# Optimization experiments

Measured on AMD Instinct MI355X. Metric: run time of the kernel, lower is better.

Reference implementation:

```python
import jax, jax.numpy as jnp
import numpy as np

B, V, F, N = 4, 8192, 16384, 8192
EPS = 1e-3        # criterion eps
WEIGHT = 1000.0   # criterion weight


def setup_inputs() -> dict:
    key = jax.random.key(0)
    k1, k2, k3 = jax.random.split(key, 3)
    pred_pos = jax.random.normal(k1, (B, N, 3), jnp.float32)
    obstacle_pos = jax.random.normal(k2, (B, V, 3), jnp.float32)
    obstacle_faces = jax.random.randint(k3, (B, F, 3), 0, V)
    return {"pred_pos": pred_pos, "obstacle_pos": obstacle_pos,
            "obstacle_faces": obstacle_faces}


def _centers_normals(pos, faces):
    # pos: [V,3], faces: [F,3] -> face centers [F,3], unit face normals [F,3]
    tri = pos[faces]                                   # [F,3,3]
    centers = tri.mean(axis=1)                         # gather(...).mean(-2)
    n = jnp.cross(tri[:, 1] - tri[:, 0], tri[:, 2] - tri[:, 0])
    n = n / jnp.maximum(jnp.linalg.norm(n, axis=-1, keepdims=True), 1e-12)
    return centers, n


def reference(pred_pos, obstacle_pos, obstacle_faces):
    centers, normals = jax.vmap(_centers_normals)(obstacle_pos, obstacle_faces)
    # brute-force 1-NN: argmin_f ||p - c_f||^2 == argmin_f (||c_f||^2 - 2 p.c_f)
    c2 = jnp.sum(centers * centers, axis=-1)                     # [B,F]
    dots = jnp.einsum('bnd,bfd->bnf', pred_pos, centers)         # [B,N,F] big
    nn_idx = jnp.argmin(c2[:, None, :] - 2.0 * dots, axis=-1)    # [B,N]
    idx3 = jnp.broadcast_to(nn_idx[:, :, None], nn_idx.shape + (3,))
    nn_points = jnp.take_along_axis(centers, idx3, axis=1)       # [B,N,3]
    nn_normals = jnp.take_along_axis(normals, idx3, axis=1)      # [B,N,3]
    distance = jnp.sum((pred_pos - nn_points) * nn_normals, axis=-1)  # [B,N]
    interp = jnp.maximum(EPS - distance, 0.0)
    perc = jnp.mean((interp > 0).astype(jnp.float32))            # mean over B of per-example means (equal N)
    loss = jnp.mean(jnp.sum(interp ** 3, axis=-1)) * WEIGHT      # sum_i loss_i / B * weight
    return loss, perc
```

## Files before the change

### kernel.cpp

```cpp
#include <hip/hip_runtime.h>
#include <cstdint>

typedef __attribute__((ext_vector_type(8))) short short8;
typedef __attribute__((ext_vector_type(4))) float floatx4;

constexpr int NB = 4;
constexpr int NV = 8192;
constexpr int NF = 16384;
constexpr int NP = 8192;
constexpr float F_EPS = 1e-3f;
constexpr float F_WEIGHT = 1000.0f;
constexpr float BIAS = 1e-3f;

constexpr int PT_TILES = NP / 16;
constexpr int FC_TILES = NF / 16;
constexpr int TPB = 256;
constexpr int TPW = 4;
constexpr int FS = 8;
constexpr int SL_TILES = FC_TILES / FS;
constexpr int CH_TILES = 32;
constexpr int NCHUNK = SL_TILES / CH_TILES;

union FragU { uint4 u; short8 s; };

__device__ inline unsigned f2bf(float f) {
    unsigned u = __float_as_uint(f);
    return (u + 0x7FFFu + ((u >> 16) & 1u)) >> 16;
}
__device__ inline float bf2f(unsigned h) { return __uint_as_float(h << 16); }
__device__ inline unsigned pk(unsigned lo, unsigned hi) {
    return (lo & 0xFFFFu) | (hi << 16);
}

__global__ void points_prep(const float* __restrict__ pred,
                            uint4* __restrict__ a_frags,
                            unsigned* __restrict__ keys,
                            float* __restrict__ acc) {
    int i = blockIdx.x * blockDim.x + threadIdx.x;
    if (i >= NB * NP) return;
    keys[i] = 0xFFFFFFFFu;
    if (i < 2) acc[i] = 0.0f;

    int b = i / NP, n = i & (NP - 1);
    float x = pred[3 * (size_t)i], y = pred[3 * (size_t)i + 1], z = pred[3 * (size_t)i + 2];
    unsigned hx = f2bf(x), hy = f2bf(y), hz = f2bf(z);
    float rx = x - bf2f(hx), ry = y - bf2f(hy), rz = z - bf2f(hz);
    unsigned ahx = f2bf(-2.f * bf2f(hx)), ahy = f2bf(-2.f * bf2f(hy)), ahz = f2bf(-2.f * bf2f(hz));
    unsigned alx = f2bf(-2.f * rx), aly = f2bf(-2.f * ry), alz = f2bf(-2.f * rz);
    float p2 = x * x + y * y + z * z + BIAS;
    unsigned p2h = f2bf(p2);
    unsigned p2l = f2bf(p2 - bf2f(p2h));
    const unsigned ONE = 0x3F80u;

    int tile = n >> 4, m = n & 15;
    uint4* base = a_frags + (size_t)(b * PT_TILES + tile) * 64;
    base[m]      = make_uint4(pk(ahx, ahy), pk(ahz, alx), pk(aly, alz), pk(ahx, ahy));
    base[16 + m] = make_uint4(pk(ahz, alx), pk(aly, alz), pk(ONE, ONE), pk(p2h, p2l));
    base[32 + m] = make_uint4(0, 0, 0, 0);
    base[48 + m] = make_uint4(0, 0, 0, 0);
}

__global__ void faces_prep(const float* __restrict__ pos,
                           const int*   __restrict__ faces,
                           uint4*  __restrict__ b_frags,
                           float4* __restrict__ centers4,
                           float4* __restrict__ normals4) {
    int i = blockIdx.x * blockDim.x + threadIdx.x;
    if (i >= NB * NF) return;
    int b = i / NF, f = i & (NF - 1);
    const float* p = pos + (size_t)b * NV * 3;
    int i0 = faces[3 * (size_t)i], i1 = faces[3 * (size_t)i + 1], i2 = faces[3 * (size_t)i + 2];
    float ax = p[3 * i0], ay = p[3 * i0 + 1], az = p[3 * i0 + 2];
    float bx = p[3 * i1], by = p[3 * i1 + 1], bz = p[3 * i1 + 2];
    float cx = p[3 * i2], cy = p[3 * i2 + 1], cz = p[3 * i2 + 2];

    const float third = 1.0f / 3.0f;
    float mx = (ax + bx + cx) * third;
    float my = (ay + by + cy) * third;
    float mz = (az + bz + cz) * third;
    float c2 = mx * mx + my * my + mz * mz;

    float e1x = bx - ax, e1y = by - ay, e1z = bz - az;
    float e2x = cx - ax, e2y = cy - ay, e2z = cz - az;
    float nx = e1y * e2z - e1z * e2y;
    float ny = e1z * e2x - e1x * e2z;
    float nz = e1x * e2y - e1y * e2x;
    float len = sqrtf(nx * nx + ny * ny + nz * nz);
    float inv = 1.0f / fmaxf(len, 1e-12f);

    centers4[i] = make_float4(mx, my, mz, c2);
    normals4[i] = make_float4(nx * inv, ny * inv, nz * inv, 0.0f);

    unsigned bhx = f2bf(mx), bhy = f2bf(my), bhz = f2bf(mz);
    unsigned blx = f2bf(mx - bf2f(bhx)), bly = f2bf(my - bf2f(bhy)), blz = f2bf(mz - bf2f(bhz));
    unsigned c2h = f2bf(c2);
    unsigned c2l = f2bf(c2 - bf2f(c2h));
    const unsigned ONE = 0x3F80u;

    int tile = f >> 4, m = f & 15;
    uint4* base = b_frags + (size_t)(b * FC_TILES + tile) * 64;
    base[m]      = make_uint4(pk(bhx, bhy), pk(bhz, bhx), pk(bhy, bhz), pk(blx, bly));
    base[16 + m] = make_uint4(pk(blz, blx), pk(bly, blz), pk(c2h, c2l), pk(ONE, ONE));
    base[32 + m] = make_uint4(0, 0, 0, 0);
    base[48 + m] = make_uint4(0, 0, 0, 0);
}

__global__ __launch_bounds__(TPB) void nn_kernel(
        const uint4* __restrict__ a_frags,
        const uint4* __restrict__ b_frags,
        unsigned* __restrict__ keys) {
    __shared__ uint4 sb[CH_TILES * 64];

    const int pg   = blockIdx.x;
    const int sl   = blockIdx.y;
    const int b    = blockIdx.z;
    const int tid  = threadIdx.x;
    const int wave = tid >> 6;
    const int lane = tid & 63;
    const int col  = lane & 15;

    FragU a[TPW];
    const int base_t = b * PT_TILES + pg * 16 + wave * TPW;
#pragma unroll
    for (int t = 0; t < TPW; ++t)
        a[t].u = a_frags[(size_t)(base_t + t) * 64 + lane];

    unsigned best[TPW * 4];
#pragma unroll
    for (int e = 0; e < TPW * 4; ++e) best[e] = 0xFFFFFFFFu;

    const floatx4 zero = {0.f, 0.f, 0.f, 0.f};

    for (int ch = 0; ch < NCHUNK; ++ch) {
        const size_t g0 = (size_t)(b * FC_TILES + sl * SL_TILES + ch * CH_TILES) * 64;
        for (int idx = tid; idx < CH_TILES * 64; idx += TPB)
            sb[idx] = b_frags[g0 + idx];
        __syncthreads();

        unsigned vface = (unsigned)(sl * (SL_TILES * 16) + ch * (CH_TILES * 16) + col);
        for (int t = 0; t < CH_TILES; ++t) {
            FragU bu;
            bu.u = sb[t * 64 + lane];
#pragma unroll
            for (int tt = 0; tt < TPW; ++tt) {
                floatx4 d = __builtin_amdgcn_mfma_f32_16x16x32_bf16(
                    a[tt].s, bu.s, zero, 0, 0, 0);
#pragma unroll
                for (int r = 0; r < 4; ++r) {
                    unsigned key = (__float_as_uint(d[r]) & 0xFFFFC000u) | vface;
                    best[tt * 4 + r] = min(best[tt * 4 + r], key);
                }
            }
            vface += 16;
        }
        __syncthreads();
    }

#pragma unroll
    for (int e = 0; e < TPW * 4; ++e) {
        unsigned v = best[e];
#pragma unroll
        for (int m = 1; m < 16; m <<= 1)
            v = min(v, (unsigned)__shfl_xor((int)v, m, 64));
        best[e] = v;
    }
    if (col == 0) {
        int q = lane >> 4;
#pragma unroll
        for (int tt = 0; tt < TPW; ++tt)
#pragma unroll
            for (int r = 0; r < 4; ++r) {
                int n = (pg * 16 + wave * TPW + tt) * 16 + q * 4 + r;
                atomicMin(&keys[b * NP + n], best[tt * 4 + r]);
            }
    }
}

__global__ __launch_bounds__(TPB) void finalize_kernel(
        const float* __restrict__ pred,
        const float4* __restrict__ centers4,
        const float4* __restrict__ normals4,
        const unsigned int* __restrict__ keys,
        float* __restrict__ acc) {
    int i = blockIdx.x * blockDim.x + threadIdx.x;
    float val = 0.0f, cnt = 0.0f;
    if (i < NB * NP) {
        int b = i / NP;
        unsigned key = keys[i];
        int idx = (int)(key & (unsigned)(NF - 1));
        float4 c  = centers4[b * NF + idx];
        float4 nr = normals4[b * NF + idx];
        const float* pp = pred + (size_t)i * 3;
        float dx = pp[0] - c.x, dy = pp[1] - c.y, dz = pp[2] - c.z;
        float dist = dx * nr.x + dy * nr.y + dz * nr.z;
        float t = F_EPS - dist;
        if (t > 0.0f) { cnt = 1.0f; val = t * t * t; }
    }
    for (int off = 32; off > 0; off >>= 1) {
        val += __shfl_down(val, off, 64);
        cnt += __shfl_down(cnt, off, 64);
    }
    __shared__ float sv[TPB / 64], sn[TPB / 64];
    int lane = threadIdx.x & 63, wave = threadIdx.x >> 6;
    if (lane == 0) { sv[wave] = val; sn[wave] = cnt; }
    __syncthreads();
    if (threadIdx.x == 0) {
        float v = 0.0f, cc = 0.0f;
#pragma unroll
        for (int w = 0; w < TPB / 64; ++w) { v += sv[w]; cc += sn[w]; }
        atomicAdd(&acc[0], v);
        atomicAdd(&acc[1], cc);
    }
}

__global__ void out_kernel(const float* __restrict__ acc,
                           float* __restrict__ out) {
    if (threadIdx.x == 0) {
        out[0] = acc[0] * (F_WEIGHT / (float)NB);
        out[1] = acc[1] * (1.0f / (float)(NB * NP));
    }
}

extern "C" void kernel_launch(void* const* d_in, const int* in_sizes, int n_in,
                              void* d_out, int out_size, void* d_ws, size_t ws_size,
                              hipStream_t stream) {
    const float* pred  = (const float*)d_in[0];
    const float* opos  = (const float*)d_in[1];
    const int*   faces = (const int*)  d_in[2];

    char* ws = (char*)d_ws;
    const size_t a_bytes = (size_t)NB * PT_TILES * 64 * 16;
    const size_t b_bytes = (size_t)NB * FC_TILES * 64 * 16;
    const size_t c_bytes = (size_t)NB * NF * 16;

    uint4*    a_frags  = (uint4*)ws;
    uint4*    b_frags  = (uint4*)(ws + a_bytes);
    float4*   centers4 = (float4*)(ws + a_bytes + b_bytes);
    float4*   normals4 = (float4*)(ws + a_bytes + b_bytes + c_bytes);
    unsigned* keys     = (unsigned*)(ws + a_bytes + b_bytes + 2 * c_bytes);
    float*    acc      = (float*)(ws + a_bytes + b_bytes + 2 * c_bytes +
                                  (size_t)NB * NP * sizeof(unsigned));

    points_prep<<<(NB * NP + TPB - 1) / TPB, TPB, 0, stream>>>(
        pred, a_frags, keys, acc);
    faces_prep<<<(NB * NF + TPB - 1) / TPB, TPB, 0, stream>>>(
        opos, faces, b_frags, centers4, normals4);

    nn_kernel<<<dim3(NP / 256, FS, NB), TPB, 0, stream>>>(
        a_frags, b_frags, keys);

    finalize_kernel<<<(NB * NP + TPB - 1) / TPB, TPB, 0, stream>>>(
        pred, centers4, normals4, keys, acc);

    out_kernel<<<1, 64, 0, stream>>>(acc, (float*)d_out);
}
```

Measured before the change: 124.1 us.

## Fuse prep kernels, drop LDS staging, fold finalize into NN kernel via tickets

```diff
diff --git a/kernel.cpp b/kernel.cpp
--- a/kernel.cpp
+++ b/kernel.cpp
@@ -16,10 +16,9 @@
 constexpr int FC_TILES = NF / 16;
 constexpr int TPB = 256;
 constexpr int TPW = 4;
-constexpr int FS = 8;
+constexpr int FS = 16;
 constexpr int SL_TILES = FC_TILES / FS;
-constexpr int CH_TILES = 32;
-constexpr int NCHUNK = SL_TILES / CH_TILES;
+constexpr int PGS = NP / 256;
 
 union FragU { uint4 u; short8 s; };
 
@@ -32,138 +31,147 @@
     return (lo & 0xFFFFu) | (hi << 16);
 }
 
-__global__ void points_prep(const float* __restrict__ pred,
+__global__ void prep_kernel(const float* __restrict__ pred,
+                            const float* __restrict__ pos,
+                            const int*   __restrict__ faces,
                             uint4* __restrict__ a_frags,
+                            uint4* __restrict__ b_frags,
+                            float4* __restrict__ centers4,
+                            float4* __restrict__ normals4,
                             unsigned* __restrict__ keys,
-                            float* __restrict__ acc) {
-    int i = blockIdx.x * blockDim.x + threadIdx.x;
-    if (i >= NB * NP) return;
-    keys[i] = 0xFFFFFFFFu;
-    if (i < 2) acc[i] = 0.0f;
-
-    int b = i / NP, n = i & (NP - 1);
-    float x = pred[3 * (size_t)i], y = pred[3 * (size_t)i + 1], z = pred[3 * (size_t)i + 2];
-    unsigned hx = f2bf(x), hy = f2bf(y), hz = f2bf(z);
-    float rx = x - bf2f(hx), ry = y - bf2f(hy), rz = z - bf2f(hz);
-    unsigned ahx = f2bf(-2.f * bf2f(hx)), ahy = f2bf(-2.f * bf2f(hy)), ahz = f2bf(-2.f * bf2f(hz));
-    unsigned alx = f2bf(-2.f * rx), aly = f2bf(-2.f * ry), alz = f2bf(-2.f * rz);
-    float p2 = x * x + y * y + z * z + BIAS;
-    unsigned p2h = f2bf(p2);
-    unsigned p2l = f2bf(p2 - bf2f(p2h));
-    const unsigned ONE = 0x3F80u;
-
-    int tile = n >> 4, m = n & 15;
-    uint4* base = a_frags + (size_t)(b * PT_TILES + tile) * 64;
-    base[m]      = make_uint4(pk(ahx, ahy), pk(ahz, alx), pk(aly, alz), pk(ahx, ahy));
-    base[16 + m] = make_uint4(pk(ahz, alx), pk(aly, alz), pk(ONE, ONE), pk(p2h, p2l));
-    base[32 + m] = make_uint4(0, 0, 0, 0);
-    base[48 + m] = make_uint4(0, 0, 0, 0);
-}
-
-__global__ void faces_prep(const float* __restrict__ pos,
-                           const int*   __restrict__ faces,
-                           uint4*  __restrict__ b_frags,
-                           float4* __restrict__ centers4,
-                           float4* __restrict__ normals4) {
+                            float* __restrict__ acc,
+                            unsigned* __restrict__ tk) {
     int i = blockIdx.x * blockDim.x + threadIdx.x;
     if (i >= NB * NF) return;
-    int b = i / NF, f = i & (NF - 1);
-    const float* p = pos + (size_t)b * NV * 3;
-    int i0 = faces[3 * (size_t)i], i1 = faces[3 * (size_t)i + 1], i2 = faces[3 * (size_t)i + 2];
-    float ax = p[3 * i0], ay = p[3 * i0 + 1], az = p[3 * i0 + 2];
-    float bx = p[3 * i1], by = p[3 * i1 + 1], bz = p[3 * i1 + 2];
-    float cx = p[3 * i2], cy = p[3 * i2 + 1], cz = p[3 * i2 + 2];
-
-    const float third = 1.0f / 3.0f;
-    float mx = (ax + bx + cx) * third;
-    float my = (ay + by + cy) * third;
-    float mz = (az + bz + cz) * third;
-    float c2 = mx * mx + my * my + mz * mz;
-
-    float e1x = bx - ax, e1y = by - ay, e1z = bz - az;
-    float e2x = cx - ax, e2y = cy - ay, e2z = cz - az;
-    float nx = e1y * e2z - e1z * e2y;
-    float ny = e1z * e2x - e1x * e2z;
-    float nz = e1x * e2y - e1y * e2x;
-    float len = sqrtf(nx * nx + ny * ny + nz * nz);
-    float inv = 1.0f / fmaxf(len, 1e-12f);
-
-    centers4[i] = make_float4(mx, my, mz, c2);
-    normals4[i] = make_float4(nx * inv, ny * inv, nz * inv, 0.0f);
-
-    unsigned bhx = f2bf(mx), bhy = f2bf(my), bhz = f2bf(mz);
-    unsigned blx = f2bf(mx - bf2f(bhx)), bly = f2bf(my - bf2f(bhy)), blz = f2bf(mz - bf2f(bhz));
-    unsigned c2h = f2bf(c2);
-    unsigned c2l = f2bf(c2 - bf2f(c2h));
+    if (i < 2) acc[i] = 0.0f;
+    if (i <= NB * PGS) tk[i] = 0u;
+
     const unsigned ONE = 0x3F80u;
 
-    int tile = f >> 4, m = f & 15;
-    uint4* base = b_frags + (size_t)(b * FC_TILES + tile) * 64;
-    base[m]      = make_uint4(pk(bhx, bhy), pk(bhz, bhx), pk(bhy, bhz), pk(blx, bly));
-    base[16 + m] = make_uint4(pk(blz, blx), pk(bly, blz), pk(c2h, c2l), pk(ONE, ONE));
-    base[32 + m] = make_uint4(0, 0, 0, 0);
-    base[48 + m] = make_uint4(0, 0, 0, 0);
-}
-
-__global__ __launch_bounds__(TPB) void nn_kernel(
+    {
+        int b = i / NF, f = i & (NF - 1);
+        const float* p = pos + (size_t)b * NV * 3;
+        int i0 = faces[3 * (size_t)i], i1 = faces[3 * (size_t)i + 1], i2 = faces[3 * (size_t)i + 2];
+        float ax = p[3 * i0], ay = p[3 * i0 + 1], az = p[3 * i0 + 2];
+        float bx = p[3 * i1], by = p[3 * i1 + 1], bz = p[3 * i1 + 2];
+        float cx = p[3 * i2], cy = p[3 * i2 + 1], cz = p[3 * i2 + 2];
+
+        const float third = 1.0f / 3.0f;
+        float mx = (ax + bx + cx) * third;
+        float my = (ay + by + cy) * third;
+        float mz = (az + bz + cz) * third;
+        float c2 = mx * mx + my * my + mz * mz;
+
+        float e1x = bx - ax, e1y = by - ay, e1z = bz - az;
+        float e2x = cx - ax, e2y = cy - ay, e2z = cz - az;
+        float nx = e1y * e2z - e1z * e2y;
+        float ny = e1z * e2x - e1x * e2z;
+        float nz = e1x * e2y - e1y * e2x;
+        float len = sqrtf(nx * nx + ny * ny + nz * nz);
+        float inv = 1.0f / fmaxf(len, 1e-12f);
+
+        centers4[i] = make_float4(mx, my, mz, c2);
+        normals4[i] = make_float4(nx * inv, ny * inv, nz * inv, 0.0f);
+
+        unsigned bhx = f2bf(mx), bhy = f2bf(my), bhz = f2bf(mz);
+        unsigned blx = f2bf(mx - bf2f(bhx)), bly = f2bf(my - bf2f(bhy)), blz = f2bf(mz - bf2f(bhz));
+        unsigned c2h = f2bf(c2);
+        unsigned c2l = f2bf(c2 - bf2f(c2h));
+
+        int tile = f >> 4, n = f & 15;
+        uint4* bb = b_frags + (size_t)(b * FC_TILES + tile) * 32;
+        bb[n]      = make_uint4(pk(bhx, bhy), pk(bhz, bhx), pk(bhy, bhz), pk(blx, bly));
+        bb[16 + n] = make_uint4(pk(blz, blx), pk(bly, blz), pk(c2h, c2l), pk(ONE, ONE));
+    }
+
+    if (i < NB * NP) {
+        keys[i] = 0xFFFFFFFFu;
+        int pb = i / NP, n = i & (NP - 1);
+        float x = pred[3 * (size_t)i], y = pred[3 * (size_t)i + 1], z = pred[3 * (size_t)i + 2];
+        unsigned hx = f2bf(x), hy = f2bf(y), hz = f2bf(z);
+        float rx = x - bf2f(hx), ry = y - bf2f(hy), rz = z - bf2f(hz);
+        unsigned ahx = f2bf(-2.f * bf2f(hx)), ahy = f2bf(-2.f * bf2f(hy)), ahz = f2bf(-2.f * bf2f(hz));
+        unsigned alx = f2bf(-2.f * rx), aly = f2bf(-2.f * ry), alz = f2bf(-2.f * rz);
+        float p2 = x * x + y * y + z * z + BIAS;
+        unsigned p2h = f2bf(p2);
+        unsigned p2l = f2bf(p2 - bf2f(p2h));
+
+        int tile = n >> 4, m = n & 15;
+        uint4* ab = a_frags + (size_t)(pb * PT_TILES + tile) * 32;
+        ab[m]      = make_uint4(pk(ahx, ahy), pk(ahz, alx), pk(aly, alz), pk(ahx, ahy));
+        ab[16 + m] = make_uint4(pk(ahz, alx), pk(aly, alz), pk(ONE, ONE), pk(p2h, p2l));
+    }
+}
+
+__global__ __launch_bounds__(TPB, 8) void nn_kernel(
+        const float* __restrict__ pred,
         const uint4* __restrict__ a_frags,
         const uint4* __restrict__ b_frags,
-        unsigned* __restrict__ keys) {
-    __shared__ uint4 sb[CH_TILES * 64];
-
-    const int pg   = blockIdx.x;
-    const int sl   = blockIdx.y;
-    const int b    = blockIdx.z;
-    const int tid  = threadIdx.x;
-    const int wave = tid >> 6;
-    const int lane = tid & 63;
-    const int col  = lane & 15;
-
-    FragU a[TPW];
+        const float4* __restrict__ centers4,
+        const float4* __restrict__ normals4,
+        unsigned* __restrict__ keys,
+        float* __restrict__ acc,
+        unsigned* __restrict__ tk,
+        float* __restrict__ out) {
+    const int pg = blockIdx.x, sl = blockIdx.y, b = blockIdx.z;
+    const int tid = threadIdx.x, wave = tid >> 6, lane = tid & 63, col = lane & 15;
+
+    __shared__ unsigned s_tkt;
+    __shared__ float sv[4], sn[4];
+
+    FragU a[TPW], b0, b1;
+    const uint4 z4 = make_uint4(0u, 0u, 0u, 0u);
+#pragma unroll
+    for (int t = 0; t < TPW; ++t) a[t].u = z4;
+    b0.u = z4; b1.u = z4;
+
     const int base_t = b * PT_TILES + pg * 16 + wave * TPW;
-#pragma unroll
-    for (int t = 0; t < TPW; ++t)
-        a[t].u = a_frags[(size_t)(base_t + t) * 64 + lane];
+    if (lane < 32) {
+#pragma unroll
+        for (int t = 0; t < TPW; ++t)
+            a[t].u = a_frags[(size_t)(base_t + t) * 32 + lane];
+    }
 
     unsigned best[TPW * 4];
 #pragma unroll
     for (int e = 0; e < TPW * 4; ++e) best[e] = 0xFFFFFFFFu;
 
     const floatx4 zero = {0.f, 0.f, 0.f, 0.f};
-
-    for (int ch = 0; ch < NCHUNK; ++ch) {
-        const size_t g0 = (size_t)(b * FC_TILES + sl * SL_TILES + ch * CH_TILES) * 64;
-        for (int idx = tid; idx < CH_TILES * 64; idx += TPB)
-            sb[idx] = b_frags[g0 + idx];
-        __syncthreads();
-
-        unsigned vface = (unsigned)(sl * (SL_TILES * 16) + ch * (CH_TILES * 16) + col);
-        for (int t = 0; t < CH_TILES; ++t) {
-            FragU bu;
-            bu.u = sb[t * 64 + lane];
-#pragma unroll
-            for (int tt = 0; tt < TPW; ++tt) {
-                floatx4 d = __builtin_amdgcn_mfma_f32_16x16x32_bf16(
-                    a[tt].s, bu.s, zero, 0, 0, 0);
-#pragma unroll
-                for (int r = 0; r < 4; ++r) {
-                    unsigned key = (__float_as_uint(d[r]) & 0xFFFFC000u) | vface;
-                    best[tt * 4 + r] = min(best[tt * 4 + r], key);
-                }
+    const uint4* bptr = b_frags + (size_t)(b * FC_TILES + sl * SL_TILES) * 32;
+    unsigned vf = (unsigned)(sl * SL_TILES * 16 + col);
+
+    for (int t = 0; t < SL_TILES; t += 2) {
+        if (lane < 32) {
+            b0.u = bptr[t * 32 + lane];
+            b1.u = bptr[t * 32 + 32 + lane];
+        }
+#pragma unroll
+        for (int tt = 0; tt < TPW; ++tt) {
+            floatx4 d0 = __builtin_amdgcn_mfma_f32_16x16x32_bf16(a[tt].s, b0.s, zero, 0, 0, 0);
+            floatx4 d1 = __builtin_amdgcn_mfma_f32_16x16x32_bf16(a[tt].s, b1.s, zero, 0, 0, 0);
+#pragma unroll
+            for (int r = 0; r < 4; ++r) {
+                unsigned k0 = (__float_as_uint(d0[r]) & 0xFFFFC000u) | vf;
+                unsigned k1 = (__float_as_uint(d1[r]) & 0xFFFFC000u) | (vf + 16u);
+                unsigned m01 = k0 < k1 ? k0 : k1;
+                unsigned bb  = best[tt * 4 + r];
+                best[tt * 4 + r] = m01 < bb ? m01 : bb;
             }
-            vface += 16;
-        }
-        __syncthreads();
+        }
+        vf += 32u;
     }
 
 #pragma unroll
     for (int e = 0; e < TPW * 4; ++e) {
         unsigned v = best[e];
 #pragma unroll
-        for (int m = 1; m < 16; m <<= 1)
-            v = min(v, (unsigned)__shfl_xor((int)v, m, 64));
+        for (int m = 1; m < 16; m <<= 1) {
+            unsigned s = (unsigned)__shfl_xor((int)v, m, 64);
+            v = s < v ? s : v;
+        }
         best[e] = v;
     }
+    unsigned* kb = keys + b * NP;
     if (col == 0) {
         int q = lane >> 4;
 #pragma unroll
@@ -171,53 +179,47 @@
 #pragma unroll
             for (int r = 0; r < 4; ++r) {
                 int n = (pg * 16 + wave * TPW + tt) * 16 + q * 4 + r;
-                atomicMin(&keys[b * NP + n], best[tt * 4 + r]);
+                atomicMin(&kb[n], best[tt * 4 + r]);
             }
     }
-}
-
-__global__ __launch_bounds__(TPB) void finalize_kernel(
-        const float* __restrict__ pred,
-        const float4* __restrict__ centers4,
-        const float4* __restrict__ normals4,
-        const unsigned int* __restrict__ keys,
-        float* __restrict__ acc) {
-    int i = blockIdx.x * blockDim.x + threadIdx.x;
-    float val = 0.0f, cnt = 0.0f;
-    if (i < NB * NP) {
-        int b = i / NP;
-        unsigned key = keys[i];
+
+    __threadfence();
+    __syncthreads();
+    if (tid == 0) s_tkt = atomicAdd(&tk[b * PGS + pg], 1u);
+    __syncthreads();
+    if (s_tkt == FS - 1) {
+        const int i = b * NP + pg * 256 + tid;
+        unsigned key = __hip_atomic_load(&keys[i], __ATOMIC_RELAXED, __HIP_MEMORY_SCOPE_AGENT);
         int idx = (int)(key & (unsigned)(NF - 1));
         float4 c  = centers4[b * NF + idx];
         float4 nr = normals4[b * NF + idx];
-        const float* pp = pred + (size_t)i * 3;
-        float dx = pp[0] - c.x, dy = pp[1] - c.y, dz = pp[2] - c.z;
+        float dx = pred[3 * (size_t)i]     - c.x;
+        float dy = pred[3 * (size_t)i + 1] - c.y;
+        float dz = pred[3 * (size_t)i + 2] - c.z;
         float dist = dx * nr.x + dy * nr.y + dz * nr.z;
-        float t = F_EPS - dist;
-        if (t > 0.0f) { cnt = 1.0f; val = t * t * t; }
-    }
-    for (int off = 32; off > 0; off >>= 1) {
-        val += __shfl_down(val, off, 64);
-        cnt += __shfl_down(cnt, off, 64);
-    }
-    __shared__ float sv[TPB / 64], sn[TPB / 64];
-    int lane = threadIdx.x & 63, wave = threadIdx.x >> 6;
-    if (lane == 0) { sv[wave] = val; sn[wave] = cnt; }
-    __syncthreads();
-    if (threadIdx.x == 0) {
-        float v = 0.0f, cc = 0.0f;
-#pragma unroll
-        for (int w = 0; w < TPB / 64; ++w) { v += sv[w]; cc += sn[w]; }
-        atomicAdd(&acc[0], v);
-        atomicAdd(&acc[1], cc);
-    }
-}
-
-__global__ void out_kernel(const float* __restrict__ acc,
-                           float* __restrict__ out) {
-    if (threadIdx.x == 0) {
-        out[0] = acc[0] * (F_WEIGHT / (float)NB);
-        out[1] = acc[1] * (1.0f / (float)(NB * NP));
+        float tpos = F_EPS - dist;
+        float val = 0.0f, cnt = 0.0f;
+        if (tpos > 0.0f) { cnt = 1.0f; val = tpos * tpos * tpos; }
+        for (int off = 32; off > 0; off >>= 1) {
+            val += __shfl_down(val, off, 64);
+            cnt += __shfl_down(cnt, off, 64);
+        }
+        if (lane == 0) { sv[wave] = val; sn[wave] = cnt; }
+        __syncthreads();
+        if (tid == 0) {
+            float v  = sv[0] + sv[1] + sv[2] + sv[3];
+            float cc = sn[0] + sn[1] + sn[2] + sn[3];
+            atomicAdd(&acc[0], v);
+            atomicAdd(&acc[1], cc);
+            __threadfence();
+            unsigned t2 = atomicAdd(&tk[NB * PGS], 1u);
+            if (t2 == (unsigned)(NB * PGS - 1)) {
+                float a0 = __hip_atomic_load(&acc[0], __ATOMIC_RELAXED, __HIP_MEMORY_SCOPE_AGENT);
+                float a1 = __hip_atomic_load(&acc[1], __ATOMIC_RELAXED, __HIP_MEMORY_SCOPE_AGENT);
+                out[0] = a0 * (F_WEIGHT / (float)NB);
+                out[1] = a1 * (1.0f / (float)(NB * NP));
+            }
+        }
     }
 }
 
@@ -229,28 +231,23 @@
     const int*   faces = (const int*)  d_in[2];
 
     char* ws = (char*)d_ws;
-    const size_t a_bytes = (size_t)NB * PT_TILES * 64 * 16;
-    const size_t b_bytes = (size_t)NB * FC_TILES * 64 * 16;
+    const size_t a_bytes = (size_t)NB * PT_TILES * 32 * 16;
+    const size_t b_bytes = (size_t)NB * FC_TILES * 32 * 16;
     const size_t c_bytes = (size_t)NB * NF * 16;
+    const size_t k_bytes = (size_t)NB * NP * sizeof(unsigned);
 
     uint4*    a_frags  = (uint4*)ws;
     uint4*    b_frags  = (uint4*)(ws + a_bytes);
     float4*   centers4 = (float4*)(ws + a_bytes + b_bytes);
     float4*   normals4 = (float4*)(ws + a_bytes + b_bytes + c_bytes);
     unsigned* keys     = (unsigned*)(ws + a_bytes + b_bytes + 2 * c_bytes);
-    float*    acc      = (float*)(ws + a_bytes + b_bytes + 2 * c_bytes +
-                                  (size_t)NB * NP * sizeof(unsigned));
-
-    points_prep<<<(NB * NP + TPB - 1) / TPB, TPB, 0, stream>>>(
-        pred, a_frags, keys, acc);
-    faces_prep<<<(NB * NF + TPB - 1) / TPB, TPB, 0, stream>>>(
-        opos, faces, b_frags, centers4, normals4);
-
-    nn_kernel<<<dim3(NP / 256, FS, NB), TPB, 0, stream>>>(
-        a_frags, b_frags, keys);
-
-    finalize_kernel<<<(NB * NP + TPB - 1) / TPB, TPB, 0, stream>>>(
-        pred, centers4, normals4, keys, acc);
-
-    out_kernel<<<1, 64, 0, stream>>>(acc, (float*)d_out);
-}
+    unsigned* tk       = (unsigned*)(ws + a_bytes + b_bytes + 2 * c_bytes + k_bytes);
+    float*    acc      = (float*)(ws + a_bytes + b_bytes + 2 * c_bytes + k_bytes +
+                                  ((size_t)(NB * PGS + 1) * sizeof(unsigned) + 15) / 16 * 16);
+
+    prep_kernel<<<(NB * NF + TPB - 1) / TPB, TPB, 0, stream>>>(
+        pred, opos, faces, a_frags, b_frags, centers4, normals4, keys, acc, tk);
+
+    nn_kernel<<<dim3(PGS, FS, NB), TPB, 0, stream>>>(
+        pred, a_frags, b_frags, centers4, normals4, keys, acc, tk, (float*)d_out);
+}
```

Result: slower. 239.2 us (+92.8%).
